# Kernel optimization log

Hardware: AMD Instinct MI355X
Metric: run time of the kernel (lower is better)

## Reference

```python
import jax, jax.numpy as jnp
import numpy as np

B, T, F, U, M = 4096, 16, 256, 512, 8
DELTA_T = 0.04

# ln_tau_table: tau = 1, 10^0.5, 10^1.0, ... -> ln(tau) = i * 0.5*ln(10)
LN_TAU = (jnp.arange(M, dtype=jnp.float32) * (0.5 * np.log(10.0))).astype(jnp.float32)
DECAY = jnp.exp(-DELTA_T / (LN_TAU + 1e-7))  # [M]


def setup_inputs() -> dict:
    key = jax.random.key(0)
    ks = jax.random.split(key, 9)
    s = lambda fan_in: 1.0 / np.sqrt(fan_in)
    return {
        "x": jax.random.normal(ks[0], (B, T, F), dtype=jnp.float32),
        "W_r": jax.random.normal(ks[1], (F + U, U * M), dtype=jnp.float32) * s(F + U),
        "b_r": jax.random.normal(ks[2], (U * M,), dtype=jnp.float32) * 0.01,
        "W_q": jax.random.normal(ks[3], (F + U, U), dtype=jnp.float32) * s(F + U),
        "b_q": jax.random.normal(ks[4], (U,), dtype=jnp.float32) * 0.01,
        "W_s": jax.random.normal(ks[5], (F + U, U * M), dtype=jnp.float32) * s(F + U),
        "b_s": jax.random.normal(ks[6], (U * M,), dtype=jnp.float32) * 0.01,
        "W_out": jax.random.normal(ks[7], (U, 3), dtype=jnp.float32) * s(U),
        "b_out": jax.random.normal(ks[8], (3,), dtype=jnp.float32) * 0.01,
    }


def _ctgru_forward(x, W_r, b_r, W_q, b_q, W_s, b_s, W_out, b_out):
    def step(h_hat, x_t):  # h_hat: [B,U,M], x_t: [B,F]
        h = h_hat.sum(axis=2)                              # [B,U]
        fused = jnp.concatenate([x_t, h], axis=1)          # [B,F+U]
        ln_tau_r = (fused @ W_r + b_r).reshape(-1, U, M)   # [B,U,M]
        r_ki = jax.nn.softmax(-jnp.square(ln_tau_r - LN_TAU), axis=2)
        q_in = jnp.concatenate([x_t, jnp.sum(r_ki * h_hat, axis=2)], axis=1)
        q_k = jnp.tanh(q_in @ W_q + b_q)[:, :, None]       # [B,U,1]
        ln_tau_s = (fused @ W_s + b_s).reshape(-1, U, M)
        s_ki = jax.nn.softmax(-jnp.square(ln_tau_s - LN_TAU), axis=2)
        h_next = ((1.0 - s_ki) * h_hat + s_ki * q_k) * DECAY
        return h_next, h_next.sum(axis=2)                  # carry, hidden [B,U]

    h0 = jnp.zeros((x.shape[0], U, M), dtype=x.dtype)
    _, hiddens = jax.lax.scan(step, h0, jnp.swapaxes(x, 0, 1))  # hiddens: [T,B,U]
    outputs = jnp.swapaxes(hiddens, 0, 1)                  # [B,T,U]
    return outputs @ W_out + b_out                         # [B,T,3]


def reference(x, W_r, b_r, W_q, b_q, W_s, b_s, W_out, b_out):
    return _ctgru_forward(x, W_r, b_r, W_q, b_q, W_s, b_s, W_out, b_out)
```

## Files before the change

### kernel.cpp

```cpp
#include <hip/hip_runtime.h>
#include <hip/hip_bf16.h>
#include <math.h>

#define B_   4096
#define T_   16
#define F_   256
#define U_   512
#define M_   8
#define K_   768
#define NRS  4096
#define NC   8192
#define LNT  1.1512925f

typedef __bf16 bf16_t;
typedef bf16_t bf16x8 __attribute__((ext_vector_type(8)));
typedef bf16_t bf16x4 __attribute__((ext_vector_type(4)));
typedef float  f32x4  __attribute__((ext_vector_type(4)));

__device__ inline void gl_lds16(const void* g, void* lds) {
    __builtin_amdgcn_global_load_lds(
        (const __attribute__((address_space(1))) unsigned int*)g,
        (__attribute__((address_space(3))) unsigned int*)lds, 16, 0, 0);
}

__global__ __launch_bounds__(256, 4) void gemm_rs_ep(
    const bf16_t* __restrict__ xt,
    const bf16_t* __restrict__ hprev,
    const bf16_t* __restrict__ Bt,
    const float*  __restrict__ biasP,
    const bf16_t* __restrict__ hhat,
    bf16_t* __restrict__ rh,
    bf16_t* __restrict__ sbuf)
{
    __shared__ bf16_t Al[2][128 * 32];
    __shared__ bf16_t Bl[2][128 * 32];

    const int tid  = threadIdx.x;
    const int lane = tid & 63;
    const int wave = tid >> 6;
    const int m0 = blockIdx.x * 128;
    const int n0 = blockIdx.y * 128;
    const int wm = (wave & 1) * 64;
    const int wn = (wave >> 1) * 64;
    const int lr = lane & 15;
    const int kq = lane >> 4;

    f32x4 acc[4][4] = {};

    const int rA0 = tid >> 2, rA1 = 64 + (tid >> 2);
    const int kc  = (tid & 3) * 8;

    for (int kk = 0; kk < K_; kk += 64) {
        const bf16_t* arow0;
        const bf16_t* arow1;
        int cbase;
        if (kk < F_) { arow0 = xt + (size_t)(m0 + rA0) * F_;
                       arow1 = xt + (size_t)(m0 + rA1) * F_; cbase = kk; }
        else         { arow0 = hprev + (size_t)(m0 + rA0) * U_;
                       arow1 = hprev + (size_t)(m0 + rA1) * U_; cbase = kk - F_; }

        __syncthreads();
        gl_lds16(arow0 + cbase + kc,      (char*)&Al[0][0] + tid * 16);
        gl_lds16(arow1 + cbase + kc,      (char*)&Al[0][0] + (tid + 256) * 16);
        gl_lds16(arow0 + cbase + 32 + kc, (char*)&Al[1][0] + tid * 16);
        gl_lds16(arow1 + cbase + 32 + kc, (char*)&Al[1][0] + (tid + 256) * 16);
        gl_lds16(Bt + (size_t)(n0 + rA0) * K_ + kk + kc,      (char*)&Bl[0][0] + tid * 16);
        gl_lds16(Bt + (size_t)(n0 + rA1) * K_ + kk + kc,      (char*)&Bl[0][0] + (tid + 256) * 16);
        gl_lds16(Bt + (size_t)(n0 + rA0) * K_ + kk + 32 + kc, (char*)&Bl[1][0] + tid * 16);
        gl_lds16(Bt + (size_t)(n0 + rA1) * K_ + kk + 32 + kc, (char*)&Bl[1][0] + (tid + 256) * 16);
        __syncthreads();

#pragma unroll
        for (int s = 0; s < 2; s++) {
            bf16x8 af[4], bfr[4];
#pragma unroll
            for (int i = 0; i < 4; i++)
                af[i] = *(const bf16x8*)(&Al[s][0] + (wm + i * 16 + lr) * 32 + kq * 8);
#pragma unroll
            for (int i = 0; i < 4; i++)
                bfr[i] = *(const bf16x8*)(&Bl[s][0] + (wn + i * 16 + lr) * 32 + kq * 8);
#pragma unroll
            for (int i = 0; i < 4; i++)
#pragma unroll
                for (int j = 0; j < 4; j++)
                    acc[i][j] = __builtin_amdgcn_mfma_f32_16x16x32_bf16(
                        af[i], bfr[j], acc[i][j], 0, 0, 0);
        }
    }

    const int nb  = n0 + wn;
    const int u3  = lane & 7;
    const int m0v = ((lane >> 3) & 1) * 4;
    const bool is_r = nb < NRS;

    float bj[4];
#pragma unroll
    for (int j = 0; j < 4; j++) bj[j] = biasP[nb + j * 16 + lr];

#pragma unroll
    for (int i = 0; i < 4; i++) {
        const int rowb = m0 + wm + i * 16 + kq * 4;
#pragma unroll
        for (int r = 0; r < 4; r++) {
            const int row = rowb + r;
            float e[4], sum = 0.f;
#pragma unroll
            for (int j = 0; j < 4; j++) {
                float v = acc[i][j][r] + bj[j];
                float d = v - (float)(m0v + j) * LNT;
                e[j] = __expf(-d * d);
                sum += e[j];
            }
            sum += __shfl_xor(sum, 8, 64);
            const float inv = 1.0f / sum;
            if (is_r) {
                bf16x4 h4 = *(const bf16x4*)(hhat + (size_t)row * NRS + nb + u3 * 8 + m0v);
                float rhv = 0.f;
#pragma unroll
                for (int j = 0; j < 4; j++) rhv += e[j] * inv * (float)h4[j];
                rhv += __shfl_xor(rhv, 8, 64);
                if ((lane & 8) == 0)
                    rh[(size_t)row * U_ + (nb >> 3) + u3] = (bf16_t)rhv;
            } else {
                bf16x4 pv;
#pragma unroll
                for (int j = 0; j < 4; j++) pv[j] = (bf16_t)(e[j] * inv);
                *(bf16x4*)(sbuf + (size_t)row * NRS + (nb - NRS) + u3 * 8 + m0v) = pv;
            }
        }
    }
}

__global__ __launch_bounds__(256) void gemm_q_up(
    const bf16_t* __restrict__ xt,
    const bf16_t* __restrict__ rh,
    const bf16_t* __restrict__ Bq,
    const float*  __restrict__ bq,
    const bf16_t* __restrict__ sbuf,
    bf16_t* __restrict__ hhat,
    bf16_t* __restrict__ hnext)
{
    __shared__ bf16_t Al[2][64 * 32];
    __shared__ bf16_t Bl[2][64 * 32];

    const int tid  = threadIdx.x;
    const int lane = tid & 63;
    const int wave = tid >> 6;
    const int m0 = blockIdx.x * 64;
    const int n0 = blockIdx.y * 64;
    const int wm = (wave & 1) * 32;
    const int wn = (wave >> 1) * 32;
    const int lr = lane & 15;
    const int kq = lane >> 4;

    f32x4 acc[2][2] = {};

    const int rA = tid >> 2;
    const int kc = (tid & 3) * 8;

    for (int kk = 0; kk < K_; kk += 64) {
        const bf16_t* arow;
        int cbase;
        if (kk < F_) { arow = xt + (size_t)(m0 + rA) * F_; cbase = kk; }
        else         { arow = rh + (size_t)(m0 + rA) * U_; cbase = kk - F_; }

        __syncthreads();
        gl_lds16(arow + cbase + kc,      (char*)&Al[0][0] + tid * 16);
        gl_lds16(arow + cbase + 32 + kc, (char*)&Al[1][0] + tid * 16);
        gl_lds16(Bq + (size_t)(n0 + rA) * K_ + kk + kc,      (char*)&Bl[0][0] + tid * 16);
        gl_lds16(Bq + (size_t)(n0 + rA) * K_ + kk + 32 + kc, (char*)&Bl[1][0] + tid * 16);
        __syncthreads();

#pragma unroll
        for (int s = 0; s < 2; s++) {
            bf16x8 af[2], bfr[2];
#pragma unroll
            for (int i = 0; i < 2; i++)
                af[i] = *(const bf16x8*)(&Al[s][0] + (wm + i * 16 + lr) * 32 + kq * 8);
#pragma unroll
            for (int i = 0; i < 2; i++)
                bfr[i] = *(const bf16x8*)(&Bl[s][0] + (wn + i * 16 + lr) * 32 + kq * 8);
#pragma unroll
            for (int i = 0; i < 2; i++)
#pragma unroll
                for (int j = 0; j < 2; j++)
                    acc[i][j] = __builtin_amdgcn_mfma_f32_16x16x32_bf16(
                        af[i], bfr[j], acc[i][j], 0, 0, 0);
        }
    }

    const float DEC[8] = {0.0f, 0.9658531f, 0.9827783f, 0.9884856f,
                          0.9913518f, 0.9930754f, 0.9942261f, 0.9950489f};

#pragma unroll
    for (int i = 0; i < 2; i++) {
        const int rowb = m0 + wm + i * 16 + kq * 4;
#pragma unroll
        for (int j = 0; j < 2; j++) {
            const int u = n0 + wn + j * 16 + lr;
            const float bv = bq[u];
#pragma unroll
            for (int r = 0; r < 4; r++) {
                const int row = rowb + r;
                const float q = tanhf(acc[i][j][r] + bv);
                const size_t base = (size_t)row * NRS + u * 8;
                bf16x8 s8 = *(const bf16x8*)(sbuf + base);
                bf16x8 h8 = *(const bf16x8*)(hhat + base);
                bf16x8 ho;
                float hs = 0.f;
#pragma unroll
                for (int m = 0; m < 8; m++) {
                    float s = (float)s8[m];
                    float h = (float)h8[m];
                    float hn = ((1.f - s) * h + s * q) * DEC[m];
                    ho[m] = (bf16_t)hn;
                    hs += hn;
                }
                *(bf16x8*)(hhat + base) = ho;
                hnext[(size_t)row * U_ + u] = (bf16_t)hs;
            }
        }
    }
}

__global__ void transpose_perm(const float* __restrict__ src, bf16_t* __restrict__ dst) {
    __shared__ float tl[32][33];
    int k0 = blockIdx.x * 32, n0 = blockIdx.y * 32;
    int tx = threadIdx.x & 31, ty = threadIdx.x >> 5;
#pragma unroll
    for (int i = 0; i < 32; i += 8)
        tl[ty + i][tx] = src[(size_t)(k0 + ty + i) * NRS + n0 + tx];
    __syncthreads();
#pragma unroll
    for (int i = 0; i < 32; i += 8) {
        int n = n0 + ty + i;
        int m = n & 7, u3v = (n >> 3) & 7;
        int p = (n & ~63) + (m & 3) * 16 + (m >> 2) * 8 + u3v;
        dst[(size_t)p * K_ + k0 + tx] = (bf16_t)tl[tx][ty + i];
    }
}

__global__ void transpose_plain(const float* __restrict__ src, bf16_t* __restrict__ dst, int N) {
    __shared__ float tl[32][33];
    int k0 = blockIdx.x * 32, n0 = blockIdx.y * 32;
    int tx = threadIdx.x & 31, ty = threadIdx.x >> 5;
#pragma unroll
    for (int i = 0; i < 32; i += 8)
        tl[ty + i][tx] = src[(size_t)(k0 + ty + i) * N + n0 + tx];
    __syncthreads();
#pragma unroll
    for (int i = 0; i < 32; i += 8)
        dst[(size_t)(n0 + ty + i) * K_ + k0 + tx] = (bf16_t)tl[tx][ty + i];
}

__global__ void bias_perm(const float* __restrict__ b_r, const float* __restrict__ b_s,
                          float* __restrict__ biasP) {
    int p = blockIdx.x * 256 + threadIdx.x;
    int pr = p & 63, j = pr >> 4, lr = pr & 15;
    int L = (p & ~63) + (lr & 7) * 8 + ((lr >> 3) & 1) * 4 + j;
    biasP[p] = (L < NRS) ? b_r[L] : b_s[L - NRS];
}

__global__ void xall_build(const float* __restrict__ x, bf16_t* __restrict__ xall) {
    int idx = blockIdx.x * 256 + threadIdx.x;
    int b = idx >> 12;
    int rem = idx & 4095;
    int t = rem >> 8, f = rem & 255;
    xall[((size_t)t * B_ + b) * F_ + f] = (bf16_t)x[idx];
}

__global__ __launch_bounds__(256) void out_all(
    const bf16_t* __restrict__ hall,
    const float* __restrict__ Wout,
    const float* __restrict__ bout,
    float* __restrict__ out)
{
    int row = blockIdx.x * 4 + (threadIdx.x >> 6);
    int lane = threadIdx.x & 63;
    bf16x8 h8 = *(const bf16x8*)(hall + (size_t)row * U_ + lane * 8);
    float p0 = 0, p1 = 0, p2 = 0;
#pragma unroll
    for (int k = 0; k < 8; k++) {
        float h = (float)h8[k];
        int u = lane * 8 + k;
        p0 += h * Wout[u * 3 + 0];
        p1 += h * Wout[u * 3 + 1];
        p2 += h * Wout[u * 3 + 2];
    }
    for (int off = 32; off; off >>= 1) {
        p0 += __shfl_down(p0, off, 64);
        p1 += __shfl_down(p1, off, 64);
        p2 += __shfl_down(p2, off, 64);
    }
    if (lane == 0) {
        int t = row >> 12, b = row & (B_ - 1);
        size_t o = ((size_t)b * T_ + t) * 3;
        out[o + 0] = p0 + bout[0];
        out[o + 1] = p1 + bout[1];
        out[o + 2] = p2 + bout[2];
    }
}

extern "C" void kernel_launch(void* const* d_in, const int* in_sizes, int n_in,
                              void* d_out, int out_size, void* d_ws, size_t ws_size,
                              hipStream_t stream) {
    const float* x   = (const float*)d_in[0];
    const float* W_r = (const float*)d_in[1];
    const float* b_r = (const float*)d_in[2];
    const float* W_q = (const float*)d_in[3];
    const float* b_q = (const float*)d_in[4];
    const float* W_s = (const float*)d_in[5];
    const float* b_s = (const float*)d_in[6];
    const float* W_o = (const float*)d_in[7];
    const float* b_o = (const float*)d_in[8];
    float* out = (float*)d_out;

    char* ws = (char*)d_ws;
    bf16_t* hhat  = (bf16_t*)ws; ws += (size_t)B_ * NRS * 2;
    bf16_t* sbuf  = (bf16_t*)ws; ws += (size_t)B_ * NRS * 2;
    bf16_t* xall  = (bf16_t*)ws; ws += (size_t)B_ * T_ * F_ * 2;
    bf16_t* hall  = (bf16_t*)ws; ws += (size_t)(T_ + 1) * B_ * U_ * 2;
    bf16_t* rh    = (bf16_t*)ws; ws += (size_t)B_ * U_ * 2;
    bf16_t* WrsT  = (bf16_t*)ws; ws += (size_t)NC * K_ * 2;
    bf16_t* WqT   = (bf16_t*)ws; ws += (size_t)U_ * K_ * 2;
    float*  biasP = (float*)ws;  ws += (size_t)NC * 4;

    hipMemsetAsync(hhat, 0, (size_t)B_ * NRS * 2, stream);
    hipMemsetAsync(hall, 0, (size_t)B_ * U_ * 2, stream);
    xall_build<<<B_ * T_ * F_ / 256, 256, 0, stream>>>(x, xall);
    transpose_perm<<<dim3(K_ / 32, NRS / 32), 256, 0, stream>>>(W_r, WrsT);
    transpose_perm<<<dim3(K_ / 32, NRS / 32), 256, 0, stream>>>(W_s, WrsT + (size_t)NRS * K_);
    transpose_plain<<<dim3(K_ / 32, U_ / 32), 256, 0, stream>>>(W_q, WqT, U_);
    bias_perm<<<NC / 256, 256, 0, stream>>>(b_r, b_s, biasP);

    for (int t = 0; t < T_; t++) {
        const bf16_t* xt = xall + (size_t)t * B_ * F_;
        const bf16_t* hp = hall + (size_t)t * B_ * U_;
        bf16_t*       hn = hall + (size_t)(t + 1) * B_ * U_;
        gemm_rs_ep<<<dim3(32, 64), 256, 0, stream>>>(xt, hp, WrsT, biasP, hhat, rh, sbuf);
        gemm_q_up<<<dim3(64, 8), 256, 0, stream>>>(xt, rh, WqT, b_q, sbuf, hhat, hn);
    }
    out_all<<<B_ * T_ / 4, 256, 0, stream>>>(hall + (size_t)B_ * U_, W_o, b_o, out);
}
```

Baseline: 1.629 ms.

## Rewrite r/s GEMM as 256x256 tile, 8-wave, multi-stage pipelined kernel

Replaces the 128x128 four-wave r/s GEMM with a 256x256 tile kernel using 512 threads. It triple-buffers K-slices in LDS through async global-to-LDS loads with explicit vmcnt waits and barriers, and applies an XOR swizzle to LDS columns to avoid bank conflicts. It also remaps block IDs for L2 locality and raises MFMA issue priority. The goal is to overlap memory loads with MFMA work and raise arithmetic intensity. The cost is higher register and LDS pressure, lower occupancy, and fragile hand-tuned wait counts.

After: 1.748 ms. +7.3%, slower.

```diff
diff --git a/kernel.cpp b/kernel.cpp
--- a/kernel.cpp
+++ b/kernel.cpp
@@ -23,7 +23,54 @@
         (__attribute__((address_space(3))) unsigned int*)lds, 16, 0, 0);
 }
 
-__global__ __launch_bounds__(256, 4) void gemm_rs_ep(
+#define VMCNT(n) asm volatile("s_waitcnt vmcnt(" #n ")" ::: "memory")
+#define LGKM0()  asm volatile("s_waitcnt lgkmcnt(0)" ::: "memory")
+#define BAR()    __builtin_amdgcn_s_barrier()
+
+__device__ inline void stageA(bf16_t* dst, const bf16_t* xt, const bf16_t* hp,
+                              int m0, int k0, int tid) {
+    const int r = tid >> 2;
+    const int c = ((tid & 3) ^ ((tid >> 3) & 3)) * 8;
+    const bf16_t *s0, *s1;
+    if (k0 < F_) {
+        s0 = xt + (size_t)(m0 + r) * F_ + k0 + c;
+        s1 = xt + (size_t)(m0 + r + 128) * F_ + k0 + c;
+    } else {
+        s0 = hp + (size_t)(m0 + r) * U_ + (k0 - F_) + c;
+        s1 = hp + (size_t)(m0 + r + 128) * U_ + (k0 - F_) + c;
+    }
+    gl_lds16(s0, (char*)dst + tid * 16);
+    gl_lds16(s1, (char*)dst + (tid + 512) * 16);
+}
+
+__device__ inline void stageB(bf16_t* dst, const bf16_t* Bt, int n0, int k0, int tid) {
+    const int r = tid >> 2;
+    const int c = ((tid & 3) ^ ((tid >> 3) & 3)) * 8;
+    gl_lds16(Bt + (size_t)(n0 + r) * K_ + k0 + c,       (char*)dst + tid * 16);
+    gl_lds16(Bt + (size_t)(n0 + r + 128) * K_ + k0 + c, (char*)dst + (tid + 512) * 16);
+}
+
+__device__ inline void ds_read4(const bf16_t* base, bf16x8 (&v)[4]) {
+    v[0] = *(const bf16x8*)(base);
+    v[1] = *(const bf16x8*)(base + 512);
+    v[2] = *(const bf16x8*)(base + 1024);
+    v[3] = *(const bf16x8*)(base + 1536);
+}
+
+template <int H>
+__device__ inline void mfma16(f32x4 (&acc)[8][4], const bf16x8 (&a)[4],
+                              const bf16x8 (&b)[4]) {
+    __builtin_amdgcn_s_setprio(1);
+#pragma unroll
+    for (int i = 0; i < 4; ++i)
+#pragma unroll
+        for (int j = 0; j < 4; ++j)
+            acc[H * 4 + i][j] = __builtin_amdgcn_mfma_f32_16x16x32_bf16(
+                a[i], b[j], acc[H * 4 + i][j], 0, 0, 0);
+    __builtin_amdgcn_s_setprio(0);
+}
+
+__global__ __launch_bounds__(512, 2) void gemm_rs_8ph(
     const bf16_t* __restrict__ xt,
     const bf16_t* __restrict__ hprev,
     const bf16_t* __restrict__ Bt,
@@ -32,81 +79,95 @@
     bf16_t* __restrict__ rh,
     bf16_t* __restrict__ sbuf)
 {
-    __shared__ bf16_t Al[2][128 * 32];
-    __shared__ bf16_t Bl[2][128 * 32];
+    __shared__ bf16_t Asl[2][2][256 * 32];
+    __shared__ bf16_t Bsl[2][2][256 * 32];
 
     const int tid  = threadIdx.x;
     const int lane = tid & 63;
     const int wave = tid >> 6;
-    const int m0 = blockIdx.x * 128;
-    const int n0 = blockIdx.y * 128;
-    const int wm = (wave & 1) * 64;
-    const int wn = (wave >> 1) * 64;
+
+    const int lin = blockIdx.y * 16 + blockIdx.x;
+    const int swz = (lin & 7) * 64 + (lin >> 3);
+    const int m0 = (swz >> 5) * 256;
+    const int n0 = (swz & 31) * 256;
+
+    const int wm = wave >> 2;
+    const int wn = wave & 3;
     const int lr = lane & 15;
     const int kq = lane >> 4;
-
-    f32x4 acc[4][4] = {};
-
-    const int rA0 = tid >> 2, rA1 = 64 + (tid >> 2);
-    const int kc  = (tid & 3) * 8;
-
-    for (int kk = 0; kk < K_; kk += 64) {
-        const bf16_t* arow0;
-        const bf16_t* arow1;
-        int cbase;
-        if (kk < F_) { arow0 = xt + (size_t)(m0 + rA0) * F_;
-                       arow1 = xt + (size_t)(m0 + rA1) * F_; cbase = kk; }
-        else         { arow0 = hprev + (size_t)(m0 + rA0) * U_;
-                       arow1 = hprev + (size_t)(m0 + rA1) * U_; cbase = kk - F_; }
-
-        __syncthreads();
-        gl_lds16(arow0 + cbase + kc,      (char*)&Al[0][0] + tid * 16);
-        gl_lds16(arow1 + cbase + kc,      (char*)&Al[0][0] + (tid + 256) * 16);
-        gl_lds16(arow0 + cbase + 32 + kc, (char*)&Al[1][0] + tid * 16);
-        gl_lds16(arow1 + cbase + 32 + kc, (char*)&Al[1][0] + (tid + 256) * 16);
-        gl_lds16(Bt + (size_t)(n0 + rA0) * K_ + kk + kc,      (char*)&Bl[0][0] + tid * 16);
-        gl_lds16(Bt + (size_t)(n0 + rA1) * K_ + kk + kc,      (char*)&Bl[0][0] + (tid + 256) * 16);
-        gl_lds16(Bt + (size_t)(n0 + rA0) * K_ + kk + 32 + kc, (char*)&Bl[1][0] + tid * 16);
-        gl_lds16(Bt + (size_t)(n0 + rA1) * K_ + kk + 32 + kc, (char*)&Bl[1][0] + (tid + 256) * 16);
-        __syncthreads();
-
-#pragma unroll
-        for (int s = 0; s < 2; s++) {
-            bf16x8 af[4], bfr[4];
-#pragma unroll
-            for (int i = 0; i < 4; i++)
-                af[i] = *(const bf16x8*)(&Al[s][0] + (wm + i * 16 + lr) * 32 + kq * 8);
-#pragma unroll
-            for (int i = 0; i < 4; i++)
-                bfr[i] = *(const bf16x8*)(&Bl[s][0] + (wn + i * 16 + lr) * 32 + kq * 8);
-#pragma unroll
-            for (int i = 0; i < 4; i++)
-#pragma unroll
-                for (int j = 0; j < 4; j++)
-                    acc[i][j] = __builtin_amdgcn_mfma_f32_16x16x32_bf16(
-                        af[i], bfr[j], acc[i][j], 0, 0, 0);
-        }
-    }
-
-    const int nb  = n0 + wn;
+    const int cr = (kq ^ ((lr >> 1) & 3)) * 8;
+
+    const int aoff0 = (wm * 128 + lr) * 32 + cr;
+    const int aoff1 = (wm * 128 + 64 + lr) * 32 + cr;
+    const int boff  = (wn * 64 + lr) * 32 + cr;
+
+    f32x4 acc[8][4] = {};
+    bf16x8 a[4], b[4];
+
+    stageA(&Asl[0][0][0], xt, hprev, m0, 0,  tid);
+    stageB(&Bsl[0][0][0], Bt, n0, 0,  tid);
+    stageA(&Asl[1][0][0], xt, hprev, m0, 32, tid);
+    stageB(&Bsl[1][0][0], Bt, n0, 32, tid);
+    stageA(&Asl[0][1][0], xt, hprev, m0, 64, tid);
+    stageB(&Bsl[0][1][0], Bt, n0, 64, tid);
+    VMCNT(8);
+    BAR();
+
+#define TILE(T, VM2, VM4, S12, S34)                                           \
+  {                                                                           \
+    const int p_ = (T) & 1, pn_ = p_ ^ 1;                                     \
+                                                                 \
+    ds_read4(&Asl[0][p_][0] + aoff0, a);                                      \
+    ds_read4(&Bsl[0][p_][0] + boff, b);                                       \
+    if (S12) stageA(&Asl[1][pn_][0], xt, hprev, m0, ((T) + 1) * 64 + 32, tid);\
+    BAR(); LGKM0();                                                           \
+    mfma16<0>(acc, a, b);                                                     \
+    BAR();                                                                    \
+                                                                 \
+    ds_read4(&Asl[0][p_][0] + aoff1, a);                                      \
+    if (S12) stageB(&Bsl[1][pn_][0], Bt, n0, ((T) + 1) * 64 + 32, tid);       \
+    VMCNT(VM2); BAR(); LGKM0();                                               \
+    mfma16<1>(acc, a, b);                                                     \
+    BAR();                                                                    \
+                                                                 \
+    ds_read4(&Asl[1][p_][0] + aoff0, a);                                      \
+    ds_read4(&Bsl[1][p_][0] + boff, b);                                       \
+    if (S34) stageA(&Asl[0][p_][0], xt, hprev, m0, ((T) + 2) * 64, tid);      \
+    BAR(); LGKM0();                                                           \
+    mfma16<0>(acc, a, b);                                                     \
+    BAR();                                                                    \
+                                                                 \
+    ds_read4(&Asl[1][p_][0] + aoff1, a);                                      \
+    if (S34) stageB(&Bsl[0][p_][0], Bt, n0, ((T) + 2) * 64, tid);             \
+    VMCNT(VM4); BAR(); LGKM0();                                               \
+    mfma16<1>(acc, a, b);                                                     \
+    BAR();                                                                    \
+  }
+
+    for (int tt = 0; tt < 10; ++tt) TILE(tt, 8, 8, 1, 1);
+    TILE(10, 8, 4, 1, 0);
+    TILE(11, 0, 0, 0, 0);
+#undef TILE
+
+    const int nb  = n0 + wn * 64;
     const int u3  = lane & 7;
     const int m0v = ((lane >> 3) & 1) * 4;
     const bool is_r = nb < NRS;
 
     float bj[4];
 #pragma unroll
-    for (int j = 0; j < 4; j++) bj[j] = biasP[nb + j * 16 + lr];
-
-#pragma unroll
-    for (int i = 0; i < 4; i++) {
-        const int rowb = m0 + wm + i * 16 + kq * 4;
-#pragma unroll
-        for (int r = 0; r < 4; r++) {
+    for (int j = 0; j < 4; ++j) bj[j] = biasP[nb + j * 16 + lr];
+
+#pragma unroll
+    for (int mi = 0; mi < 8; ++mi) {
+        const int rowb = m0 + wm * 128 + mi * 16 + kq * 4;
+#pragma unroll
+        for (int r = 0; r < 4; ++r) {
             const int row = rowb + r;
             float e[4], sum = 0.f;
 #pragma unroll
-            for (int j = 0; j < 4; j++) {
-                float v = acc[i][j][r] + bj[j];
+            for (int j = 0; j < 4; ++j) {
+                float v = acc[mi][j][r] + bj[j];
                 float d = v - (float)(m0v + j) * LNT;
                 e[j] = __expf(-d * d);
                 sum += e[j];
@@ -117,14 +178,14 @@
                 bf16x4 h4 = *(const bf16x4*)(hhat + (size_t)row * NRS + nb + u3 * 8 + m0v);
                 float rhv = 0.f;
 #pragma unroll
-                for (int j = 0; j < 4; j++) rhv += e[j] * inv * (float)h4[j];
+                for (int j = 0; j < 4; ++j) rhv += e[j] * inv * (float)h4[j];
                 rhv += __shfl_xor(rhv, 8, 64);
                 if ((lane & 8) == 0)
                     rh[(size_t)row * U_ + (nb >> 3) + u3] = (bf16_t)rhv;
             } else {
                 bf16x4 pv;
 #pragma unroll
-                for (int j = 0; j < 4; j++) pv[j] = (bf16_t)(e[j] * inv);
+                for (int j = 0; j < 4; ++j) pv[j] = (bf16_t)(e[j] * inv);
                 *(bf16x4*)(sbuf + (size_t)row * NRS + (nb - NRS) + u3 * 8 + m0v) = pv;
             }
         }
@@ -337,7 +398,7 @@
         const bf16_t* xt = xall + (size_t)t * B_ * F_;
         const bf16_t* hp = hall + (size_t)t * B_ * U_;
         bf16_t*       hn = hall + (size_t)(t + 1) * B_ * U_;
-        gemm_rs_ep<<<dim3(32, 64), 256, 0, stream>>>(xt, hp, WrsT, biasP, hhat, rh, sbuf);
+        gemm_rs_8ph<<<dim3(16, 32), 512, 0, stream>>>(xt, hp, WrsT, biasP, hhat, rh, sbuf);
         gemm_q_up<<<dim3(64, 8), 256, 0, stream>>>(xt, rh, WqT, b_q, sbuf, hhat, hn);
     }
     out_all<<<B_ * T_ / 4, 256, 0, stream>>>(hall + (size_t)B_ * U_, W_o, b_o, out);
```
